# Optimization experiments

Measured on AMD Instinct MI355X. Metric: run time of the kernel, lower is better.

The kernel has to match this reference:

```python
import jax, jax.numpy as jnp
import numpy as np

EPS = 1e-5

def _conv1x1(x, w, b):
    # x: (b,c,h,w), w: (o,c) -> (b,o,h,w)
    return jnp.einsum('bchw,oc->bohw', x, w) + b[None, :, None, None]

def _maxpool2(x):
    b, c, h, w = x.shape
    return x.reshape(b, c, h // 2, 2, w // 2, 2).max(axis=(3, 5))

def setup_inputs() -> dict:
    key = jax.random.key(0)
    ks = jax.random.split(key, 11)
    C, CI, H, W, B = 256, 128, 64, 64, 8
    s = 0.05
    return {
        'x': jax.random.normal(ks[0], (B, C, H, W), jnp.float32),
        'Wg': jax.random.normal(ks[1], (CI, C), jnp.float32) * s,
        'bg': jax.random.normal(ks[2], (CI,), jnp.float32) * s,
        'Wt': jax.random.normal(ks[3], (CI, C), jnp.float32) * s,
        'bt': jax.random.normal(ks[4], (CI,), jnp.float32) * s,
        'Wp': jax.random.normal(ks[5], (CI, C), jnp.float32) * s,
        'bp': jax.random.normal(ks[6], (CI,), jnp.float32) * s,
        'Ww': jax.random.normal(ks[7], (C, CI), jnp.float32) * s,
        'bw': jax.random.normal(ks[8], (C,), jnp.float32) * s,
        'gamma': jax.random.normal(ks[9], (C,), jnp.float32),
        'beta': jax.random.normal(ks[10], (C,), jnp.float32),
    }

def reference(x, Wg, bg, Wt, bt, Wp, bp, Ww, bw, gamma, beta):
    b, C, H, W = x.shape
    CI = Wg.shape[0]
    # g and phi are sub-sampled by 2x2 max pool -> M = (H/2)*(W/2); theta keeps N = H*W
    g_x = _maxpool2(_conv1x1(x, Wg, bg)).reshape(b, CI, -1).transpose(0, 2, 1)   # (b,M,ci)
    theta_x = _conv1x1(x, Wt, bt).reshape(b, CI, -1).transpose(0, 2, 1)          # (b,N,ci)
    phi_x = _maxpool2(_conv1x1(x, Wp, bp)).reshape(b, CI, -1)                    # (b,ci,M)
    f = jnp.einsum('bnc,bcm->bnm', theta_x, phi_x)                               # (b,N,M)
    f_div_C = jax.nn.softmax(f, axis=-1)
    y = jnp.einsum('bnm,bmc->bnc', f_div_C, g_x)                                 # (b,N,ci)
    y = y.transpose(0, 2, 1).reshape(b, CI, H, W)
    # W: 1x1 conv + BatchNorm2d (training mode: batch statistics, biased var)
    wy = _conv1x1(y, Ww, bw)
    mean = wy.mean(axis=(0, 2, 3), keepdims=True)
    var = ((wy - mean) ** 2).mean(axis=(0, 2, 3), keepdims=True)
    wy = (wy - mean) * jax.lax.rsqrt(var + EPS)
    wy = wy * gamma[None, :, None, None] + beta[None, :, None, None]
    z = wy + x
    # self.avg_pool is AdaptiveMaxPool2d(1): global spatial max
    return z.max(axis=(2, 3), keepdims=True)
```

## Files before the change

### kernel.cpp

```cpp
#include <hip/hip_runtime.h>
#include <hip/hip_bf16.h>
#include <stdint.h>

using f32x4  = __attribute__((ext_vector_type(4))) float;
using bf16x8 = __attribute__((ext_vector_type(8))) short;
using short4v = __attribute__((ext_vector_type(4))) short;

#define DEVINL static __device__ __forceinline__

DEVINL short f2bf(float f) {
    union { float f; uint32_t u; } v; v.f = f;
    uint32_t r = (v.u + 0x7FFFu + ((v.u >> 16) & 1u)) >> 16;
    return (short)(uint16_t)r;
}
DEVINL float bf2f(short s) {
    union { uint32_t u; float f; } v; v.u = ((uint32_t)(uint16_t)s) << 16;
    return v.f;
}
DEVINL float fexp2(float x) {
    float r;
    asm("v_exp_f32 %0, %1" : "=v"(r) : "v"(x));
    return r;
}

DEVINL void gld16(const short* g, short* l) {
    __builtin_amdgcn_global_load_lds(
        (const __attribute__((address_space(1))) unsigned int*)g,
        (__attribute__((address_space(3))) unsigned int*)l, 16, 0, 0);
}

#define LOG2E 1.44269504f

__global__ __launch_bounds__(256) void k0_prep(
        const float* __restrict__ Wg, const float* __restrict__ Wt, const float* __restrict__ Wp,
        const float* __restrict__ bg, const float* __restrict__ bt, const float* __restrict__ bp,
        const float* __restrict__ Ww,
        short* __restrict__ W_all, short* __restrict__ Ww16, float* __restrict__ b_all,
        float* __restrict__ stats) {
    int i = blockIdx.x * 256 + threadIdx.x;
    if (blockIdx.x == 0) {
        stats[threadIdx.x] = 0.f;
        stats[threadIdx.x + 256] = 0.f;
    }
    if (i < 384 * 256) {
        int r = i >> 8, c = i & 255;
        float v = (r < 128) ? Wg[r * 256 + c]
                : (r < 256) ? Wt[(r - 128) * 256 + c] * LOG2E
                            : Wp[(r - 256) * 256 + c];
        W_all[i] = f2bf(v);
    } else if (i < 384 * 256 + 256 * 128) {
        int j = i - 384 * 256;
        Ww16[j] = f2bf(Ww[j]);
    }
    if (i < 384) {
        b_all[i] = (i < 128) ? bg[i] : (i < 256) ? bt[i - 128] * LOG2E : bp[i - 256];
    }
}

__global__ __launch_bounds__(256) void k1_conv(const float* __restrict__ x,
        const short* __restrict__ W_all, const float* __restrict__ b_all,
        short* __restrict__ OutT, short* __restrict__ Kmat, short* __restrict__ Vmat) {
    __shared__ short xs[128 * 32];
    __shared__ short obuf[128 * 128];
    const int ntile = blockIdx.x;
    const int otile = blockIdx.y;
    const int b     = blockIdx.z;
    const int tid  = threadIdx.x;
    const int lane = tid & 63;
    const int wave = tid >> 6;
    const int wn = wave >> 1, wo = wave & 1;
    const int l15 = lane & 15, lh = lane >> 4;

    f32x4 acc[4][4];
    #pragma unroll
    for (int i = 0; i < 4; i++)
        #pragma unroll
        for (int j = 0; j < 4; j++) acc[i][j] = f32x4{0.f, 0.f, 0.f, 0.f};

    const int n0 = ntile * 128;
    const int ob = otile * 128 + wo * 64;
    const float* xb = x + (size_t)b * 256 * 4096;

    const int srow_base = (lane & 15) + wave * 16;
    const int sc0 = (lane >> 4) * 8;

    for (int kt = 0; kt < 8; kt++) {
        __syncthreads();
        #pragma unroll
        for (int p = 0; p < 2; p++) {
            int row = srow_base + p * 64;
            const float* xp = xb + (size_t)(kt * 32 + sc0) * 4096 + n0 + row;
            bf16x8 w8;
            #pragma unroll
            for (int j = 0; j < 8; j++) w8[j] = f2bf(xp[(size_t)j * 4096]);
            int ch = (sc0 >> 3) ^ ((row >> 1) & 3);
            *(bf16x8*)&xs[row * 32 + ch * 8] = w8;
        }
        __syncthreads();

        bf16x8 a[4], w[4];
        #pragma unroll
        for (int nf = 0; nf < 4; nf++) {
            int row = wn * 64 + nf * 16 + l15;
            int ch  = lh ^ ((row >> 1) & 3);
            a[nf] = *(const bf16x8*)&xs[row * 32 + ch * 8];
        }
        #pragma unroll
        for (int of = 0; of < 4; of++)
            w[of] = *(const bf16x8*)(W_all + (size_t)(ob + of * 16 + l15) * 256 + kt * 32 + lh * 8);
        #pragma unroll
        for (int nf = 0; nf < 4; nf++)
            #pragma unroll
            for (int of = 0; of < 4; of++)
                acc[nf][of] = __builtin_amdgcn_mfma_f32_16x16x32_bf16(a[nf], w[of], acc[nf][of], 0, 0, 0);
    }

    #pragma unroll
    for (int of = 0; of < 4; of++) {
        int ocol = wo * 64 + of * 16 + l15;
        float bias = b_all[otile * 128 + ocol];
        #pragma unroll
        for (int nf = 0; nf < 4; nf++)
            #pragma unroll
            for (int r = 0; r < 4; r++) {
                int n  = wn * 64 + nf * 16 + lh * 4 + r;
                int ch = (ocol >> 3) ^ (n & 15);
                obuf[n * 128 + ch * 8 + (ocol & 7)] = f2bf(acc[nf][of][r] + bias);
            }
    }
    __syncthreads();

    if (otile == 1) {
        #pragma unroll
        for (int p = 0; p < 8; p++) {
            int n  = wave * 4 + lh + p * 16;
            int ch = l15 ^ (n & 15);
            bf16x8 v = *(const bf16x8*)&obuf[n * 128 + ch * 8];
            *(bf16x8*)(OutT + ((size_t)b * 4096 + n0 + n) * 128 + l15 * 8) = v;
        }
    } else if (otile == 2) {
        const int wp = tid >> 3;
        const int cc = (tid & 7) * 16;
        short* kdst = Kmat + ((size_t)b * 1024 + ntile * 32 + wp) * 128 + cc;
        #pragma unroll
        for (int cblk = 0; cblk < 2; cblk++) {
            const int chunk = (cc >> 3) + cblk;
            float mx[8];
            #pragma unroll
            for (int j = 0; j < 8; j++) mx[j] = -1e30f;
            #pragma unroll
            for (int q4 = 0; q4 < 4; q4++) {
                int n = (q4 >> 1) * 64 + 2 * wp + (q4 & 1);
                bf16x8 v = *(const bf16x8*)&obuf[n * 128 + ((chunk ^ (n & 15)) * 8)];
                #pragma unroll
                for (int j = 0; j < 8; j++) mx[j] = fmaxf(mx[j], bf2f(v[j]));
            }
            bf16x8 vo;
            #pragma unroll
            for (int j = 0; j < 8; j++) vo[j] = f2bf(mx[j]);
            *(bf16x8*)(kdst + cblk * 8) = vo;
        }
    } else {
        const int c   = tid >> 1;
        const int wp0 = (tid & 1) * 16;
        const int chb = c >> 3, cl = c & 7;
        #pragma unroll
        for (int half = 0; half < 2; half++) {
            bf16x8 vo;
            #pragma unroll
            for (int j = 0; j < 8; j++) {
                int wp = wp0 + half * 8 + j;
                float mx = -1e30f;
                #pragma unroll
                for (int q4 = 0; q4 < 4; q4++) {
                    int n = (q4 >> 1) * 64 + 2 * wp + (q4 & 1);
                    mx = fmaxf(mx, bf2f(obuf[n * 128 + ((chb ^ (n & 15)) * 8) + cl]));
                }
                vo[j] = f2bf(mx);
            }
            *(bf16x8*)(Vmat + ((size_t)b * 128 + c) * 1024 + ntile * 32 + wp0 + half * 8) = vo;
        }
    }
}

__global__ __launch_bounds__(256) void k3_attn(const short* __restrict__ OutT,
        const short* __restrict__ Kmat, const short* __restrict__ Vmat,
        short* __restrict__ Ybuf) {
    __shared__ short sK[2][64 * 128];
    __shared__ short sV[2][128 * 64];
    __shared__ short sP[4][16 * 64];

    const int bid = blockIdx.x;
    const int b   = bid & 7;
    const int nt  = bid >> 3;
    const int tid = threadIdx.x;
    const int lane = tid & 63;
    const int wave = tid >> 6;
    const int l15 = lane & 15, lh = lane >> 4;
    const int n0 = nt * 64 + wave * 16;

    const short* Kb = Kmat + (size_t)b * 1024 * 128;
    const short* Vb = Vmat + (size_t)b * 128 * 1024;
    short* sPw = sP[wave];

    auto STAGE = [&](int t, int bufi) {
        const int m0 = t * 64;
        #pragma unroll
        for (int i = 0; i < 4; i++) {
            const int segb = (i * 4 + wave) * 64;
            const int rowK = (segb >> 4) + (lane >> 4);
            const int chkK = lane & 15;
            gld16(Kb + (size_t)(m0 + rowK) * 128 + ((chkK ^ (rowK & 15)) << 3),
                  &sK[bufi][segb * 8]);
            const int rowV = (segb >> 3) + (lane >> 3);
            const int chkV = lane & 7;
            gld16(Vb + (size_t)rowV * 1024 + m0 + ((chkV ^ (rowV & 7)) << 3),
                  &sV[bufi][segb * 8]);
        }
    };

    bf16x8 q[4];
    {
        const short* qrow = OutT + ((size_t)b * 4096 + n0 + l15) * 128;
        #pragma unroll
        for (int ks = 0; ks < 4; ks++)
            q[ks] = *(const bf16x8*)(qrow + ks * 32 + lh * 8);
    }

    f32x4 y[8];
    #pragma unroll
    for (int cf = 0; cf < 8; cf++) y[cf] = f32x4{0.f, 0.f, 0.f, 0.f};
    float mrun = -1e30f, lrun = 0.f;

    STAGE(0, 0);
    int cur = 0;

    for (int t = 0; t < 16; t++) {
        if (t < 15) {
            STAGE(t + 1, cur ^ 1);
            asm volatile("s_waitcnt vmcnt(8)" ::: "memory");
        } else {
            asm volatile("s_waitcnt vmcnt(0)" ::: "memory");
        }
        __builtin_amdgcn_s_barrier();
        __builtin_amdgcn_sched_barrier(0);

        const short* cK = sK[cur];
        const short* cV = sV[cur];

        f32x4 S[4];
        #pragma unroll
        for (int mf = 0; mf < 4; mf++) S[mf] = f32x4{0.f, 0.f, 0.f, 0.f};
        #pragma unroll
        for (int ks = 0; ks < 4; ks++) {
            bf16x8 kf[4];
            #pragma unroll
            for (int mf = 0; mf < 4; mf++) {
                int mrow = mf * 16 + l15;
                int jj   = ks * 4 + lh;
                kf[mf] = *(const bf16x8*)&cK[mrow * 128 + ((jj ^ (mrow & 15)) << 3)];
            }
            __builtin_amdgcn_s_setprio(1);
            #pragma unroll
            for (int mf = 0; mf < 4; mf++)
                S[mf] = __builtin_amdgcn_mfma_f32_16x16x32_bf16(kf[mf], q[ks], S[mf], 0, 0, 0);
            __builtin_amdgcn_s_setprio(0);
        }

        float pm = S[0][0];
        #pragma unroll
        for (int mf = 0; mf < 4; mf++)
            #pragma unroll
            for (int r = 0; r < 4; r++) pm = fmaxf(pm, S[mf][r]);
        pm = fmaxf(pm, __shfl_xor(pm, 16));
        pm = fmaxf(pm, __shfl_xor(pm, 32));

        if (__any(pm > mrun + 8.656f)) {
            float mnew  = fmaxf(mrun, pm);
            float alpha = fexp2(mrun - mnew);
            mrun = mnew;
            lrun *= alpha;
            float aR[4];
            #pragma unroll
            for (int r = 0; r < 4; r++) aR[r] = __shfl(alpha, lh * 4 + r);
            #pragma unroll
            for (int cf = 0; cf < 8; cf++)
                #pragma unroll
                for (int r = 0; r < 4; r++) y[cf][r] *= aR[r];
        }
        float rs = 0.f;
        #pragma unroll
        for (int mf = 0; mf < 4; mf++)
            #pragma unroll
            for (int r = 0; r < 4; r++) {
                float p = fexp2(S[mf][r] - mrun);
                S[mf][r] = p;
                rs += p;
            }
        rs += __shfl_xor(rs, 16);
        rs += __shfl_xor(rs, 32);
        lrun += rs;

        #pragma unroll
        for (int mf = 0; mf < 4; mf++) {
            short4v pk = { f2bf(S[mf][0]), f2bf(S[mf][1]), f2bf(S[mf][2]), f2bf(S[mf][3]) };
            *(short4v*)&sPw[(l15 << 6) + (((mf * 4 + lh) ^ l15) << 2)] = pk;
        }

        #pragma unroll
        for (int ks2 = 0; ks2 < 2; ks2++) {
            int u0 = ks2 * 8 + lh * 2;
            short4v lo = *(const short4v*)&sPw[(l15 << 6) + (((u0)     ^ l15) << 2)];
            short4v hi = *(const short4v*)&sPw[(l15 << 6) + (((u0 + 1) ^ l15) << 2)];
            bf16x8 pa = { lo.x, lo.y, lo.z, lo.w, hi.x, hi.y, hi.z, hi.w };
            int jj = ks2 * 4 + lh;
            __builtin_amdgcn_s_setprio(1);
            #pragma unroll
            for (int cf = 0; cf < 8; cf++) {
                int crow = cf * 16 + l15;
                bf16x8 vf = *(const bf16x8*)&cV[crow * 64 + ((jj ^ (crow & 7)) << 3)];
                y[cf] = __builtin_amdgcn_mfma_f32_16x16x32_bf16(pa, vf, y[cf], 0, 0, 0);
            }
            __builtin_amdgcn_s_setprio(0);
        }

        __builtin_amdgcn_sched_barrier(0);
        __builtin_amdgcn_s_barrier();
        cur ^= 1;
    }

    float linv[4];
    #pragma unroll
    for (int r = 0; r < 4; r++) linv[r] = 1.f / __shfl(lrun, lh * 4 + r);
    #pragma unroll
    for (int cf = 0; cf < 8; cf++) {
        int c = cf * 16 + l15;
        #pragma unroll
        for (int r = 0; r < 4; r++)
            Ybuf[((size_t)b * 4096 + n0 + lh * 4 + r) * 128 + c] = f2bf(y[cf][r] * linv[r]);
    }
}

__global__ __launch_bounds__(256) void k4_wy(const short* __restrict__ Ww16,
        const short* __restrict__ Ybuf, const float* __restrict__ bw,
        short* __restrict__ wy, float* __restrict__ stats) {
    __shared__ float sums[4][64][2];
    const int nt = blockIdx.x;
    const int ot = blockIdx.y;
    const int b  = blockIdx.z;
    const int tid = threadIdx.x;
    const int lane = tid & 63, wave = tid >> 6;
    const int l15 = lane & 15, lh = lane >> 4;
    const int ob = ot * 64;
    const int nb = nt * 256 + wave * 64;

    bf16x8 aw[4][4];
    #pragma unroll
    for (int of = 0; of < 4; of++)
        #pragma unroll
        for (int ks = 0; ks < 4; ks++)
            aw[of][ks] = *(const bf16x8*)(Ww16 + (size_t)(ob + of * 16 + l15) * 128 + ks * 32 + lh * 8);

    f32x4 acc[4][4];
    #pragma unroll
    for (int i = 0; i < 4; i++)
        #pragma unroll
        for (int j = 0; j < 4; j++) acc[i][j] = f32x4{0.f, 0.f, 0.f, 0.f};

    #pragma unroll
    for (int nf = 0; nf < 4; nf++) {
        bf16x8 by[4];
        #pragma unroll
        for (int ks = 0; ks < 4; ks++)
            by[ks] = *(const bf16x8*)(Ybuf + ((size_t)b * 4096 + nb + nf * 16 + l15) * 128 + ks * 32 + lh * 8);
        #pragma unroll
        for (int of = 0; of < 4; of++)
            #pragma unroll
            for (int ks = 0; ks < 4; ks++)
                acc[of][nf] = __builtin_amdgcn_mfma_f32_16x16x32_bf16(aw[of][ks], by[ks], acc[of][nf], 0, 0, 0);
    }

    #pragma unroll
    for (int of = 0; of < 4; of++) {
        #pragma unroll
        for (int r = 0; r < 4; r++) {
            int o = ob + of * 16 + lh * 4 + r;
            float bias = bw[o];
            float s = 0.f, s2 = 0.f;
            #pragma unroll
            for (int nf = 0; nf < 4; nf++) {
                float v = acc[of][nf][r] + bias;
                wy[((size_t)b * 256 + o) * 4096 + nb + nf * 16 + l15] = f2bf(v);
                s += v; s2 += v * v;
            }
            #pragma unroll
            for (int off = 1; off < 16; off <<= 1) { s += __shfl_xor(s, off); s2 += __shfl_xor(s2, off); }
            if (l15 == 0) {
                sums[wave][of * 16 + lh * 4 + r][0] = s;
                sums[wave][of * 16 + lh * 4 + r][1] = s2;
            }
        }
    }
    __syncthreads();
    if (tid < 64) {
        float s  = sums[0][tid][0] + sums[1][tid][0] + sums[2][tid][0] + sums[3][tid][0];
        float s2 = sums[0][tid][1] + sums[1][tid][1] + sums[2][tid][1] + sums[3][tid][1];
        atomicAdd(&stats[(ob + tid) * 2], s);
        atomicAdd(&stats[(ob + tid) * 2 + 1], s2);
    }
}

__global__ __launch_bounds__(256) void k5_bnmax(const short* __restrict__ wy,
        const float* __restrict__ x, const float* __restrict__ stats,
        const float* __restrict__ gamma, const float* __restrict__ beta,
        float* __restrict__ outp) {
    int b = blockIdx.x >> 8;
    int o = blockIdx.x & 255;
    int tid = threadIdx.x;
    float mean = stats[o * 2] * (1.f / 32768.f);
    float var  = stats[o * 2 + 1] * (1.f / 32768.f) - mean * mean;
    float rstd = rsqrtf(var + 1e-5f);
    float A = rstd * gamma[o];
    float B = beta[o] - mean * A;
    const short* pw = wy + ((size_t)b * 256 + o) * 4096;
    const float* px = x + ((size_t)b * 256 + o) * 4096;
    float mx = -1e30f;
    #pragma unroll
    for (int j = 0; j < 2; j++) {
        int e = (tid + j * 256) * 8;
        bf16x8 w8 = *(const bf16x8*)(pw + e);
        float4 xa = *(const float4*)(px + e);
        float4 xb = *(const float4*)(px + e + 4);
        mx = fmaxf(mx, bf2f(w8[0]) * A + B + xa.x);
        mx = fmaxf(mx, bf2f(w8[1]) * A + B + xa.y);
        mx = fmaxf(mx, bf2f(w8[2]) * A + B + xa.z);
        mx = fmaxf(mx, bf2f(w8[3]) * A + B + xa.w);
        mx = fmaxf(mx, bf2f(w8[4]) * A + B + xb.x);
        mx = fmaxf(mx, bf2f(w8[5]) * A + B + xb.y);
        mx = fmaxf(mx, bf2f(w8[6]) * A + B + xb.z);
        mx = fmaxf(mx, bf2f(w8[7]) * A + B + xb.w);
    }
    #pragma unroll
    for (int off = 1; off < 64; off <<= 1) mx = fmaxf(mx, __shfl_xor(mx, off));
    __shared__ float red[4];
    if ((tid & 63) == 0) red[tid >> 6] = mx;
    __syncthreads();
    if (tid == 0)
        outp[b * 256 + o] = fmaxf(fmaxf(red[0], red[1]), fmaxf(red[2], red[3]));
}

extern "C" void kernel_launch(void* const* d_in, const int* in_sizes, int n_in,
                              void* d_out, int out_size, void* d_ws, size_t ws_size,
                              hipStream_t stream) {
    const float* x     = (const float*)d_in[0];
    const float* Wg    = (const float*)d_in[1];
    const float* bg    = (const float*)d_in[2];
    const float* Wt    = (const float*)d_in[3];
    const float* bt    = (const float*)d_in[4];
    const float* Wp    = (const float*)d_in[5];
    const float* bp    = (const float*)d_in[6];
    const float* Ww    = (const float*)d_in[7];
    const float* bw    = (const float*)d_in[8];
    const float* gamma = (const float*)d_in[9];
    const float* beta  = (const float*)d_in[10];
    float* outp = (float*)d_out;

    char* ws = (char*)d_ws;
    size_t off = 0;
    auto alloc = [&](size_t bytes) -> void* {
        void* p = ws + off;
        off = (off + bytes + 255) & ~(size_t)255;
        return p;
    };
    short* W_all = (short*)alloc((size_t)384 * 256 * 2);
    short* Ww16  = (short*)alloc((size_t)256 * 128 * 2);
    float* b_all = (float*)alloc((size_t)384 * 4);
    short* OutT  = (short*)alloc((size_t)8 * 4096 * 128 * 2);
    short* Kmat  = (short*)alloc((size_t)8 * 1024 * 128 * 2);
    short* Vmat  = (short*)alloc((size_t)8 * 128 * 1024 * 2);
    short* Ybuf  = (short*)alloc((size_t)8 * 4096 * 128 * 2);
    short* wy    = (short*)alloc((size_t)8 * 256 * 4096 * 2);
    float* stats = (float*)alloc((size_t)256 * 2 * 4);

    k0_prep<<<512, 256, 0, stream>>>(Wg, Wt, Wp, bg, bt, bp, Ww, W_all, Ww16, b_all, stats);
    k1_conv<<<dim3(32, 3, 8), 256, 0, stream>>>(x, W_all, b_all, OutT, Kmat, Vmat);
    k3_attn<<<512, 256, 0, stream>>>(OutT, Kmat, Vmat, Ybuf);
    k4_wy<<<dim3(16, 4, 8), 256, 0, stream>>>(Ww16, Ybuf, bw, wy, stats);
    k5_bnmax<<<2048, 256, 0, stream>>>(wy, x, stats, gamma, beta, outp);
}
```

Baseline: 100.2 us.

## Fuse W projection into attention epilogue and compute BN stats separately

The attention kernel now normalizes its output tile, reshuffles it through shared memory into MFMA operand layout, and multiplies it directly by the W 1x1-conv weights. It writes wy itself, so the Ybuf intermediate and the separate k4_wy GEMM kernel are gone. BatchNorm statistics move to a new per-channel reduction kernel that re-reads wy and writes the sums without atomics, so stats no longer need zeroing. This removes one round trip through global memory and one launch. In exchange, every attention block reloads all W weights, the attention epilogue grows, and there is an extra full pass over wy to compute the stats.

```diff
diff --git a/kernel.cpp b/kernel.cpp
--- a/kernel.cpp
+++ b/kernel.cpp
@@ -35,13 +35,8 @@
         const float* __restrict__ Wg, const float* __restrict__ Wt, const float* __restrict__ Wp,
         const float* __restrict__ bg, const float* __restrict__ bt, const float* __restrict__ bp,
         const float* __restrict__ Ww,
-        short* __restrict__ W_all, short* __restrict__ Ww16, float* __restrict__ b_all,
-        float* __restrict__ stats) {
+        short* __restrict__ W_all, short* __restrict__ Ww16, float* __restrict__ b_all) {
     int i = blockIdx.x * 256 + threadIdx.x;
-    if (blockIdx.x == 0) {
-        stats[threadIdx.x] = 0.f;
-        stats[threadIdx.x + 256] = 0.f;
-    }
     if (i < 384 * 256) {
         int r = i >> 8, c = i & 255;
         float v = (r < 128) ? Wg[r * 256 + c]
@@ -185,7 +180,8 @@
 
 __global__ __launch_bounds__(256) void k3_attn(const short* __restrict__ OutT,
         const short* __restrict__ Kmat, const short* __restrict__ Vmat,
-        short* __restrict__ Ybuf) {
+        const short* __restrict__ Ww16, const float* __restrict__ bw,
+        short* __restrict__ wy) {
     __shared__ short sK[2][64 * 128];
     __shared__ short sV[2][128 * 64];
     __shared__ short sP[4][16 * 64];
@@ -332,81 +328,73 @@
     float linv[4];
     #pragma unroll
     for (int r = 0; r < 4; r++) linv[r] = 1.f / __shfl(lrun, lh * 4 + r);
-    #pragma unroll
-    for (int cf = 0; cf < 8; cf++) {
-        int c = cf * 16 + l15;
-        #pragma unroll
-        for (int r = 0; r < 4; r++)
-            Ybuf[((size_t)b * 4096 + n0 + lh * 4 + r) * 128 + c] = f2bf(y[cf][r] * linv[r]);
-    }
-}
-
-__global__ __launch_bounds__(256) void k4_wy(const short* __restrict__ Ww16,
-        const short* __restrict__ Ybuf, const float* __restrict__ bw,
-        short* __restrict__ wy, float* __restrict__ stats) {
-    __shared__ float sums[4][64][2];
-    const int nt = blockIdx.x;
-    const int ot = blockIdx.y;
-    const int b  = blockIdx.z;
+
+    bf16x8 by[4];
+    #pragma unroll
+    for (int h = 0; h < 2; h++) {
+        #pragma unroll
+        for (int cfl = 0; cfl < 4; cfl++) {
+            int cf = h * 4 + cfl;
+            #pragma unroll
+            for (int r = 0; r < 4; r++) {
+                int n = lh * 4 + r;
+                int chunk4 = cfl * 4 + (l15 >> 2);
+                sPw[n * 64 + ((chunk4 ^ n) << 2) + (l15 & 3)] = f2bf(y[cf][r] * linv[r]);
+            }
+        }
+        #pragma unroll
+        for (int ks2 = 0; ks2 < 2; ks2++) {
+            int u0 = ks2 * 8 + lh * 2;
+            short4v lo = *(const short4v*)&sPw[(l15 << 6) + (((u0)     ^ l15) << 2)];
+            short4v hi = *(const short4v*)&sPw[(l15 << 6) + (((u0 + 1) ^ l15) << 2)];
+            by[h * 2 + ks2] = bf16x8{ lo.x, lo.y, lo.z, lo.w, hi.x, hi.y, hi.z, hi.w };
+        }
+    }
+
+    #pragma unroll
+    for (int of = 0; of < 16; of++) {
+        bf16x8 aw[4];
+        #pragma unroll
+        for (int ks = 0; ks < 4; ks++)
+            aw[ks] = *(const bf16x8*)(Ww16 + (size_t)(of * 16 + l15) * 128 + ks * 32 + lh * 8);
+        f32x4 acc = f32x4{0.f, 0.f, 0.f, 0.f};
+        #pragma unroll
+        for (int ks = 0; ks < 4; ks++)
+            acc = __builtin_amdgcn_mfma_f32_16x16x32_bf16(aw[ks], by[ks], acc, 0, 0, 0);
+        #pragma unroll
+        for (int r = 0; r < 4; r++) {
+            int o = of * 16 + lh * 4 + r;
+            wy[((size_t)b * 256 + o) * 4096 + n0 + l15] = f2bf(acc[r] + bw[o]);
+        }
+    }
+}
+
+__global__ __launch_bounds__(256) void k4s_stats(const short* __restrict__ wy,
+        float* __restrict__ stats) {
+    const int o = blockIdx.x;
     const int tid = threadIdx.x;
-    const int lane = tid & 63, wave = tid >> 6;
-    const int l15 = lane & 15, lh = lane >> 4;
-    const int ob = ot * 64;
-    const int nb = nt * 256 + wave * 64;
-
-    bf16x8 aw[4][4];
-    #pragma unroll
-    for (int of = 0; of < 4; of++)
-        #pragma unroll
-        for (int ks = 0; ks < 4; ks++)
-            aw[of][ks] = *(const bf16x8*)(Ww16 + (size_t)(ob + of * 16 + l15) * 128 + ks * 32 + lh * 8);
-
-    f32x4 acc[4][4];
-    #pragma unroll
-    for (int i = 0; i < 4; i++)
-        #pragma unroll
-        for (int j = 0; j < 4; j++) acc[i][j] = f32x4{0.f, 0.f, 0.f, 0.f};
-
-    #pragma unroll
-    for (int nf = 0; nf < 4; nf++) {
-        bf16x8 by[4];
-        #pragma unroll
-        for (int ks = 0; ks < 4; ks++)
-            by[ks] = *(const bf16x8*)(Ybuf + ((size_t)b * 4096 + nb + nf * 16 + l15) * 128 + ks * 32 + lh * 8);
-        #pragma unroll
-        for (int of = 0; of < 4; of++)
-            #pragma unroll
-            for (int ks = 0; ks < 4; ks++)
-                acc[of][nf] = __builtin_amdgcn_mfma_f32_16x16x32_bf16(aw[of][ks], by[ks], acc[of][nf], 0, 0, 0);
-    }
-
-    #pragma unroll
-    for (int of = 0; of < 4; of++) {
-        #pragma unroll
-        for (int r = 0; r < 4; r++) {
-            int o = ob + of * 16 + lh * 4 + r;
-            float bias = bw[o];
-            float s = 0.f, s2 = 0.f;
-            #pragma unroll
-            for (int nf = 0; nf < 4; nf++) {
-                float v = acc[of][nf][r] + bias;
-                wy[((size_t)b * 256 + o) * 4096 + nb + nf * 16 + l15] = f2bf(v);
-                s += v; s2 += v * v;
-            }
-            #pragma unroll
-            for (int off = 1; off < 16; off <<= 1) { s += __shfl_xor(s, off); s2 += __shfl_xor(s2, off); }
-            if (l15 == 0) {
-                sums[wave][of * 16 + lh * 4 + r][0] = s;
-                sums[wave][of * 16 + lh * 4 + r][1] = s2;
-            }
-        }
-    }
+    float s = 0.f, s2 = 0.f;
+    #pragma unroll
+    for (int b = 0; b < 8; b++) {
+        const short* p = wy + ((size_t)b * 256 + o) * 4096;
+        #pragma unroll
+        for (int i = 0; i < 2; i++) {
+            bf16x8 v = *(const bf16x8*)(p + (tid + i * 256) * 8);
+            #pragma unroll
+            for (int j = 0; j < 8; j++) {
+                float f = bf2f(v[j]);
+                s += f; s2 += f * f;
+            }
+        }
+    }
+    #pragma unroll
+    for (int off = 1; off < 64; off <<= 1) { s += __shfl_xor(s, off); s2 += __shfl_xor(s2, off); }
+    __shared__ float red[4][2];
+    if ((tid & 63) == 0) { red[tid >> 6][0] = s; red[tid >> 6][1] = s2; }
     __syncthreads();
-    if (tid < 64) {
-        float s  = sums[0][tid][0] + sums[1][tid][0] + sums[2][tid][0] + sums[3][tid][0];
-        float s2 = sums[0][tid][1] + sums[1][tid][1] + sums[2][tid][1] + sums[3][tid][1];
-        atomicAdd(&stats[(ob + tid) * 2], s);
-        atomicAdd(&stats[(ob + tid) * 2 + 1], s2);
+    if (tid == 0) {
+        stats[o * 2]     = red[0][0] + red[1][0] + red[2][0] + red[3][0];
+        stats[o * 2 + 1] = red[0][1] + red[1][1] + red[2][1] + red[3][1];
     }
 }
 
@@ -478,13 +466,12 @@
     short* OutT  = (short*)alloc((size_t)8 * 4096 * 128 * 2);
     short* Kmat  = (short*)alloc((size_t)8 * 1024 * 128 * 2);
     short* Vmat  = (short*)alloc((size_t)8 * 128 * 1024 * 2);
-    short* Ybuf  = (short*)alloc((size_t)8 * 4096 * 128 * 2);
     short* wy    = (short*)alloc((size_t)8 * 256 * 4096 * 2);
     float* stats = (float*)alloc((size_t)256 * 2 * 4);
 
-    k0_prep<<<512, 256, 0, stream>>>(Wg, Wt, Wp, bg, bt, bp, Ww, W_all, Ww16, b_all, stats);
+    k0_prep<<<512, 256, 0, stream>>>(Wg, Wt, Wp, bg, bt, bp, Ww, W_all, Ww16, b_all);
     k1_conv<<<dim3(32, 3, 8), 256, 0, stream>>>(x, W_all, b_all, OutT, Kmat, Vmat);
-    k3_attn<<<512, 256, 0, stream>>>(OutT, Kmat, Vmat, Ybuf);
-    k4_wy<<<dim3(16, 4, 8), 256, 0, stream>>>(Ww16, Ybuf, bw, wy, stats);
+    k3_attn<<<512, 256, 0, stream>>>(OutT, Kmat, Vmat, Ww16, bw, wy);
+    k4s_stats<<<256, 256, 0, stream>>>(wy, stats);
     k5_bnmax<<<2048, 256, 0, stream>>>(wy, x, stats, gamma, beta, outp);
 }
```

After: 97.55 us. -2.6%, faster.
